# Kernel tuning notes

Hardware: AMD Instinct MI355X
Metric: run time of the kernel (lower is better)

The kernel has to match this reference:

```python
import jax, jax.numpy as jnp
import numpy as np

BATCH, SEQ, D_IN, D_OUT = 32, 1024, 128, 128
NEG_SLOPE = 0.1


def setup_inputs() -> dict:
    key = jax.random.key(0)
    k1, k2, k3, k4 = jax.random.split(key, 4)
    nodes = jax.random.normal(k1, (BATCH, SEQ, D_IN), dtype=jnp.float32)
    adjacent = jax.random.randint(k2, (BATCH, SEQ, SEQ), 0, 2, dtype=jnp.int32)
    W = jax.random.normal(k3, (D_IN, D_OUT), dtype=jnp.float32) / np.sqrt(D_IN)
    B = jax.random.normal(k4, (D_IN, D_OUT), dtype=jnp.float32) / np.sqrt(D_IN)
    return {"nodes": nodes, "adjacent": adjacent, "W": W, "B": B}


def reference(nodes, adjacent, W, B):
    # mask[b, out, in] = 1 if edge (out -> in) present
    mask = (adjacent != 0).astype(nodes.dtype)
    # counts[b, in] = in-degree (number of 'out' neighbors pooled per target node)
    counts = mask.sum(axis=1)                               # [b, s_in]
    # segment-sum of neighbor features: pooled[b, in, d] = sum_out mask * nodes[b, out, d]
    pooled = jnp.einsum('boi,bod->bid', mask, nodes)        # [b, s_in, d]
    # mean over neighbors; nodes with zero degree get no pooled contribution
    pooled = jnp.where(counts[..., None] > 0,
                       pooled / jnp.maximum(counts, 1.0)[..., None],
                       jnp.zeros((), dtype=nodes.dtype))
    updated = nodes @ B + pooled @ W                        # [b, s, d_out]
    return jax.nn.leaky_relu(updated, negative_slope=NEG_SLOPE)
```

## Files before the change

kernel.cpp:

```cpp
#include <hip/hip_runtime.h>
#include <hip/hip_bf16.h>

#define SEQ 1024
#define DIM 128
#define NEG_SLOPE 0.1f

typedef __bf16 bf16x8 __attribute__((ext_vector_type(8)));
typedef float f32x4v __attribute__((ext_vector_type(4)));

__device__ __forceinline__ unsigned short bfb(float f) {
    __bf16 h = (__bf16)f;
    return __builtin_bit_cast(unsigned short, h);
}
__device__ __forceinline__ unsigned mpack(int x0, int x1) {
    unsigned m0 = (x0 != 0) ? 0x3F80u : 0u;
    unsigned m1 = (x1 != 0) ? 0x3F80u : 0u;
    return m0 | (m1 << 16);
}
__device__ __forceinline__ int fxv(int x) {
    return ((x & 3) | ((x & 1) << 2)) ^ ((x >> 2) & 7);
}
__device__ __forceinline__ void bar() {
    asm volatile("s_waitcnt lgkmcnt(0)" ::: "memory");
    __builtin_amdgcn_s_barrier();
    __builtin_amdgcn_sched_barrier(0);
}

__global__ __launch_bounds__(256)
void wb_t(const float* __restrict__ W, const float* __restrict__ Bm,
          unsigned short* __restrict__ WT, unsigned short* __restrict__ BT) {
    const int gid = blockIdx.x * 256 + threadIdx.x;
    const int n = gid >> 7, k = gid & 127;
    WT[gid] = bfb(W[k * DIM + n]);
    BT[gid] = bfb(Bm[k * DIM + n]);
}

__global__ __launch_bounds__(256)
void nodes_t_kernel(const float* __restrict__ nodes, unsigned short* __restrict__ nodesT) {
    const int b  = blockIdx.x >> 4;
    const int o0 = (blockIdx.x & 15) << 6;
    __shared__ unsigned short T[DIM][66];

    const float* src = nodes + (size_t)b * SEQ * DIM;
    const int t = threadIdx.x & 31;
    const int g = threadIdx.x >> 5;

    float4 v[8];
    #pragma unroll
    for (int r = 0; r < 8; ++r)
        v[r] = *(const float4*)(src + (size_t)(o0 + g * 8 + r) * DIM + 4 * t);
    #pragma unroll
    for (int j = 0; j < 4; ++j) {
        #pragma unroll
        for (int p = 0; p < 4; ++p) {
            unsigned w = (unsigned)bfb(((const float*)&v[2 * p])[j]) |
                         ((unsigned)bfb(((const float*)&v[2 * p + 1])[j]) << 16);
            *(unsigned*)((unsigned char*)&T[0][0] + (size_t)(4 * t + j) * 132 + (g * 8 + 2 * p) * 2) = w;
        }
    }
    __syncthreads();
    const int d = threadIdx.x >> 1, h = threadIdx.x & 1;
    unsigned u[16];
    #pragma unroll
    for (int s = 0; s < 16; ++s)
        u[s] = *(const unsigned*)((const unsigned char*)&T[0][0] + (size_t)d * 132 + h * 64 + s * 4);
    unsigned short* dst = nodesT + (size_t)b * DIM * SEQ + (size_t)d * SEQ + o0 + h * 32;
    #pragma unroll
    for (int s = 0; s < 4; ++s) {
        uint4 q = make_uint4(u[4 * s], u[4 * s + 1], u[4 * s + 2], u[4 * s + 3]);
        *(uint4*)((unsigned char*)dst + s * 16) = q;
    }
}

__global__ __launch_bounds__(256, 4)
void gcn_fused(const float* __restrict__ nodes,
               const int* __restrict__ adj,
               const unsigned short* __restrict__ nodesT,
               const unsigned short* __restrict__ WT,
               const unsigned short* __restrict__ BT,
               float* __restrict__ out)
{
    __shared__ union {
        unsigned char  m[2][4096];
        unsigned short pooled[32][136];
    } u;

    const int bid   = blockIdx.x;
    const int xcd   = bid & 7;
    const int slot  = bid >> 3;
    const int batch = ((slot >> 5) << 3) | xcd;
    const int itile = slot & 31;
    const int i0    = itile << 5;

    const int tid  = threadIdx.x;
    const int wave = tid >> 6;
    const int lane = tid & 63;
    const int lrow = lane & 15;
    const int quad = lane >> 4;

    const int*            __restrict__ adj_b   = adj    + (size_t)batch * SEQ * SEQ;
    const float*          __restrict__ nodes_b = nodes  + (size_t)batch * SEQ * DIM;
    const unsigned short* __restrict__ nT_b    = nodesT + (size_t)batch * DIM * SEQ;

    const int tq   = tid >> 3;
    const int ic   = tid & 7;
    const int fxic = fxv(ic);
    const int gi0  = i0 + 4 * ic;
    const int o0   = 2 * tq;

    const int fx0 = fxv(lrow >> 2);
    const int fx1 = fxv(4 + (lrow >> 2));

    f32x4v acc[2][2] = {};
    f32x4v acc_cnt[2] = {};
    bf16x8 ones;
    #pragma unroll
    for (int j = 0; j < 8; ++j) ones[j] = __builtin_bit_cast(__bf16, (unsigned short)0x3F80);

    int4   A0[2], A1[2];
    bf16x8 bvA[4], bvB[4];

    auto load_adj = [&](int c, int4 (&A)[2]) {
        const int* pa = adj_b + (size_t)(c * 64 + o0) * SEQ + gi0;
        A[0] = *(const int4*)pa;
        A[1] = *(const int4*)(pa + SEQ);
    };
    auto load_bv = [&](int c, bf16x8 (&bv)[4]) {
        const unsigned short* pn = nT_b + (size_t)(wave * 32 + lrow) * SEQ + c * 64 + quad * 8;
        bv[0] = *(const bf16x8*)(pn);
        bv[1] = *(const bf16x8*)(pn + 16 * SEQ);
        bv[2] = *(const bf16x8*)(pn + 32);
        bv[3] = *(const bf16x8*)(pn + 16 * SEQ + 32);
    };
    auto write_mask = [&](int b, const int4 (&A)[2]) {
        unsigned char* mb = u.m[b];
        #pragma unroll
        for (int j = 0; j < 4; ++j) {
            unsigned w = mpack(((const int*)&A[0])[j], ((const int*)&A[1])[j]);
            *(unsigned*)(mb + (4 * ic + j) * 128 + (((tq >> 2) ^ fxic) << 4) + 4 * (tq & 3)) = w;
        }
    };
    auto compute = [&](int b, const bf16x8 (&bv)[4]) {
        const unsigned char* mb = u.m[b];
        #pragma unroll
        for (int kk = 0; kk < 2; ++kk) {
            bf16x8 av0 = *(const bf16x8*)(mb + lrow * 128        + (((4 * kk + quad) ^ fx0) << 4));
            bf16x8 av1 = *(const bf16x8*)(mb + (16 + lrow) * 128 + (((4 * kk + quad) ^ fx1) << 4));
            acc[0][0] = __builtin_amdgcn_mfma_f32_16x16x32_bf16(av0, bv[2 * kk + 0], acc[0][0], 0, 0, 0);
            acc[0][1] = __builtin_amdgcn_mfma_f32_16x16x32_bf16(av0, bv[2 * kk + 1], acc[0][1], 0, 0, 0);
            acc[1][0] = __builtin_amdgcn_mfma_f32_16x16x32_bf16(av1, bv[2 * kk + 0], acc[1][0], 0, 0, 0);
            acc[1][1] = __builtin_amdgcn_mfma_f32_16x16x32_bf16(av1, bv[2 * kk + 1], acc[1][1], 0, 0, 0);
            acc_cnt[0] = __builtin_amdgcn_mfma_f32_16x16x32_bf16(av0, ones, acc_cnt[0], 0, 0, 0);
            acc_cnt[1] = __builtin_amdgcn_mfma_f32_16x16x32_bf16(av1, ones, acc_cnt[1], 0, 0, 0);
        }
    };

    load_adj(0, A0); load_adj(1, A1);
    load_bv(0, bvA); load_bv(1, bvB);
    write_mask(0, A0);
    load_adj(2, A0);
    bar();

    for (int cc = 0; cc < 8; ++cc) {
        const int c0 = 2 * cc;
        compute(0, bvA);
        write_mask(1, A1);
        if (c0 + 3 < 16) load_adj(c0 + 3, A1);
        if (c0 + 2 < 16) load_bv(c0 + 2, bvA);
        bar();
        compute(1, bvB);
        if (c0 + 2 < 16) write_mask(0, A0);
        if (c0 + 4 < 16) load_adj(c0 + 4, A0);
        if (c0 + 3 < 16) load_bv(c0 + 3, bvB);
        bar();
    }

    #pragma unroll
    for (int mf = 0; mf < 2; ++mf) {
        #pragma unroll
        for (int r = 0; r < 4; ++r) {
            const int row = mf * 16 + quad * 4 + r;
            const float cnt = acc_cnt[mf][r];
            const float inv = (cnt > 0.5f) ? 1.0f / cnt : 0.0f;
            #pragma unroll
            for (int nf = 0; nf < 2; ++nf)
                u.pooled[row][wave * 32 + nf * 16 + lrow] = bfb(acc[mf][nf][r] * inv);
        }
    }
    bar();

    f32x4v acc2[2][2] = {};
    const int dn = wave * 32 + lrow;

    #pragma unroll
    for (int ks = 0; ks < 4; ++ks) {
        const int k0 = ks * 32 + quad * 8;
        bf16x8 av[2], bv2[2];
        #pragma unroll
        for (int mf = 0; mf < 2; ++mf)
            av[mf] = *(const bf16x8*)((const unsigned char*)&u.pooled[0][0] + (mf * 16 + lrow) * 272 + k0 * 2);
        #pragma unroll
        for (int nf = 0; nf < 2; ++nf)
            bv2[nf] = *(const bf16x8*)(WT + (size_t)(dn + nf * 16) * DIM + k0);
        #pragma unroll
        for (int mf = 0; mf < 2; ++mf)
            #pragma unroll
            for (int nf = 0; nf < 2; ++nf)
                acc2[mf][nf] = __builtin_amdgcn_mfma_f32_16x16x32_bf16(av[mf], bv2[nf], acc2[mf][nf], 0, 0, 0);
    }
    #pragma unroll
    for (int ks = 0; ks < 4; ++ks) {
        const int k0 = ks * 32 + quad * 8;
        bf16x8 av[2], bv2[2];
        #pragma unroll
        for (int mf = 0; mf < 2; ++mf) {
            const float* p = nodes_b + (size_t)(i0 + mf * 16 + lrow) * DIM + k0;
            const float4 f1 = *(const float4*)p;
            const float4 f2 = *(const float4*)(p + 4);
            av[mf][0] = (__bf16)f1.x; av[mf][1] = (__bf16)f1.y;
            av[mf][2] = (__bf16)f1.z; av[mf][3] = (__bf16)f1.w;
            av[mf][4] = (__bf16)f2.x; av[mf][5] = (__bf16)f2.y;
            av[mf][6] = (__bf16)f2.z; av[mf][7] = (__bf16)f2.w;
        }
        #pragma unroll
        for (int nf = 0; nf < 2; ++nf)
            bv2[nf] = *(const bf16x8*)(BT + (size_t)(dn + nf * 16) * DIM + k0);
        #pragma unroll
        for (int mf = 0; mf < 2; ++mf)
            #pragma unroll
            for (int nf = 0; nf < 2; ++nf)
                acc2[mf][nf] = __builtin_amdgcn_mfma_f32_16x16x32_bf16(av[mf], bv2[nf], acc2[mf][nf], 0, 0, 0);
    }

    float* out_b = out + (size_t)batch * SEQ * DIM;
    #pragma unroll
    for (int mf = 0; mf < 2; ++mf) {
        #pragma unroll
        for (int nf = 0; nf < 2; ++nf) {
            const int col = wave * 32 + nf * 16 + lrow;
            #pragma unroll
            for (int r = 0; r < 4; ++r) {
                const int row = i0 + mf * 16 + quad * 4 + r;
                const float x = acc2[mf][nf][r];
                out_b[(size_t)row * DIM + col] = (x > 0.0f) ? x : NEG_SLOPE * x;
            }
        }
    }
}

#define BUF_STRIDE 24576
#define NODES_OFF  8192
__device__ __forceinline__ int fb_swz(int row, int unit) {
    const int x  = row >> 2;
    const int fx = ((x & 3) | ((x & 1) << 2)) ^ ((x >> 2) & 7);
    return row * 128 + ((unit ^ fx) << 4);
}
__global__ __launch_bounds__(256, 2)
void gcn_fused_fb(const float* __restrict__ nodes, const int* __restrict__ adj,
                  const float* __restrict__ W, const float* __restrict__ Bm,
                  float* __restrict__ out)
{
    __shared__ alignas(16) unsigned char lds[2 * BUF_STRIDE];
    const int bid = blockIdx.x, xcd = bid & 7, slot = bid >> 3;
    const int batch = ((slot >> 4) << 3) | xcd, mtile = slot & 15, i0 = mtile << 6;
    const int tid = threadIdx.x, wave = tid >> 6, lane = tid & 63;
    const int wm = wave >> 1, wn = wave & 1, lrow = lane & 15, quad = lane >> 4;
    const int* __restrict__ adj_b = adj + (size_t)batch * SEQ * SEQ;
    const float* __restrict__ nodes_b = nodes + (size_t)batch * SEQ * DIM;
    const int a_row = (tid >> 4) * 4, a_col = (tid & 15) * 4;
    const int n_row = (tid >> 5) * 4, n_col = (tid & 31) * 4;
    const int m_unit = (tid >> 4) >> 1, m_sub = ((tid >> 4) & 1) * 8;
    const int n_unit = (tid >> 5) >> 1, n_sub = ((tid >> 5) & 1) * 8;
    f32x4v acc[2][4] = {}; f32x4v acc_cnt[2] = {};
    bf16x8 ones;
    #pragma unroll
    for (int j = 0; j < 8; ++j) ones[j] = __builtin_bit_cast(__bf16, (unsigned short)0x3F80);
    int4 A0[4], A1[4]; float4 N0[8], N1[8];
    auto load_chunk = [&](int o0, int4 (&A)[4], float4 (&N)[8]) {
        const int* pa = adj_b + (size_t)(o0 + a_row) * SEQ + (i0 + a_col);
        #pragma unroll
        for (int r = 0; r < 4; ++r) A[r] = *(const int4*)(pa + (size_t)r * SEQ);
        const float* pn = nodes_b + (size_t)(o0 + n_row) * DIM + n_col;
        #pragma unroll
        for (int it = 0; it < 2; ++it)
            #pragma unroll
            for (int r = 0; r < 4; ++r)
                N[it * 4 + r] = *(const float4*)(pn + (size_t)(it * 32 + r) * DIM);
    };
    auto write_lds = [&](int base, const int4 (&A)[4], const float4 (&N)[8]) {
        unsigned char* mb = lds + base; unsigned char* nb = lds + base + NODES_OFF;
        #pragma unroll
        for (int j = 0; j < 4; ++j) {
            uint2 w;
            w.x = mpack(((const int*)&A[0])[j], ((const int*)&A[1])[j]);
            w.y = mpack(((const int*)&A[2])[j], ((const int*)&A[3])[j]);
            *(uint2*)(mb + fb_swz(a_col + j, m_unit) + m_sub) = w;
        }
        #pragma unroll
        for (int it = 0; it < 2; ++it) {
            #pragma unroll
            for (int j = 0; j < 4; ++j) {
                uint2 w;
                w.x = (unsigned)bfb(((const float*)&N[it*4+0])[j]) | ((unsigned)bfb(((const float*)&N[it*4+1])[j]) << 16);
                w.y = (unsigned)bfb(((const float*)&N[it*4+2])[j]) | ((unsigned)bfb(((const float*)&N[it*4+3])[j]) << 16);
                *(uint2*)(nb + fb_swz(n_col + j, 4 * it + n_unit) + n_sub) = w;
            }
        }
    };
    auto compute = [&](int base) {
        const unsigned char* mb = lds + base; const unsigned char* nb = lds + base + NODES_OFF;
        #pragma unroll
        for (int kk = 0; kk < 2; ++kk) {
            bf16x8 av[2], bv[4];
            av[0] = *(const bf16x8*)(mb + fb_swz(wm * 32 + lrow, 4 * kk + quad));
            av[1] = *(const bf16x8*)(mb + fb_swz(wm * 32 + 16 + lrow, 4 * kk + quad));
            #pragma unroll
            for (int nf = 0; nf < 4; ++nf)
                bv[nf] = *(const bf16x8*)(nb + fb_swz(wn * 64 + nf * 16 + lrow, 4 * kk + quad));
            #pragma unroll
            for (int mf = 0; mf < 2; ++mf) {
                #pragma unroll
                for (int nf = 0; nf < 4; ++nf)
                    acc[mf][nf] = __builtin_amdgcn_mfma_f32_16x16x32_bf16(av[mf], bv[nf], acc[mf][nf], 0, 0, 0);
                acc_cnt[mf] = __builtin_amdgcn_mfma_f32_16x16x32_bf16(av[mf], ones, acc_cnt[mf], 0, 0, 0);
            }
        }
    };
    load_chunk(0, A0, N0); load_chunk(64, A1, N1);
    write_lds(0, A0, N0); load_chunk(128, A0, N0); bar();
    for (int cc = 0; cc < 8; ++cc) {
        const int c0 = cc * 2;
        compute(0); write_lds(BUF_STRIDE, A1, N1);
        if (c0 + 3 < 16) load_chunk((c0 + 3) * 64, A1, N1);
        bar();
        compute(BUF_STRIDE);
        if (c0 + 2 < 16) write_lds(0, A0, N0);
        if (c0 + 4 < 16) load_chunk((c0 + 4) * 64, A0, N0);
        bar();
    }
    unsigned short (*pooled)[136] = (unsigned short (*)[136])(void*)lds;
    #pragma unroll
    for (int mf = 0; mf < 2; ++mf)
        #pragma unroll
        for (int r = 0; r < 4; ++r) {
            const int row = wm * 32 + mf * 16 + quad * 4 + r;
            const float cnt = acc_cnt[mf][r];
            const float inv = (cnt > 0.5f) ? 1.0f / cnt : 0.0f;
            #pragma unroll
            for (int nf = 0; nf < 4; ++nf)
                pooled[row][wn * 64 + nf * 16 + lrow] = bfb(acc[mf][nf][r] * inv);
        }
    __syncthreads();
    f32x4v acc2[2][4] = {};
    const int d_b0 = wn * 64 + lrow;
    #pragma unroll
    for (int ks = 0; ks < 4; ++ks) {
        const int k0 = ks * 32 + quad * 8;
        bf16x8 av[2];
        #pragma unroll
        for (int mf = 0; mf < 2; ++mf)
            av[mf] = *(const bf16x8*)&pooled[wm * 32 + mf * 16 + lrow][k0];
        bf16x8 bv[4];
        const float* pw = W + (size_t)k0 * DIM + d_b0;
        #pragma unroll
        for (int nf = 0; nf < 4; ++nf)
            #pragma unroll
            for (int j = 0; j < 8; ++j) bv[nf][j] = (__bf16)pw[j * DIM + nf * 16];
        #pragma unroll
        for (int mf = 0; mf < 2; ++mf)
            #pragma unroll
            for (int nf = 0; nf < 4; ++nf)
                acc2[mf][nf] = __builtin_amdgcn_mfma_f32_16x16x32_bf16(av[mf], bv[nf], acc2[mf][nf], 0, 0, 0);
    }
    #pragma unroll
    for (int ks = 0; ks < 4; ++ks) {
        const int k0 = ks * 32 + quad * 8;
        bf16x8 av[2];
        #pragma unroll
        for (int mf = 0; mf < 2; ++mf) {
            const float* p = nodes_b + (size_t)(i0 + wm * 32 + mf * 16 + lrow) * DIM + k0;
            const float4 f1 = *(const float4*)p; const float4 f2 = *(const float4*)(p + 4);
            av[mf][0] = (__bf16)f1.x; av[mf][1] = (__bf16)f1.y;
            av[mf][2] = (__bf16)f1.z; av[mf][3] = (__bf16)f1.w;
            av[mf][4] = (__bf16)f2.x; av[mf][5] = (__bf16)f2.y;
            av[mf][6] = (__bf16)f2.z; av[mf][7] = (__bf16)f2.w;
        }
        bf16x8 bv[4];
        const float* pB = Bm + (size_t)k0 * DIM + d_b0;
        #pragma unroll
        for (int nf = 0; nf < 4; ++nf)
            #pragma unroll
            for (int j = 0; j < 8; ++j) bv[nf][j] = (__bf16)pB[j * DIM + nf * 16];
        #pragma unroll
        for (int mf = 0; mf < 2; ++mf)
            #pragma unroll
            for (int nf = 0; nf < 4; ++nf)
                acc2[mf][nf] = __builtin_amdgcn_mfma_f32_16x16x32_bf16(av[mf], bv[nf], acc2[mf][nf], 0, 0, 0);
    }
    float* out_b = out + (size_t)batch * SEQ * DIM;
    #pragma unroll
    for (int mf = 0; mf < 2; ++mf)
        #pragma unroll
        for (int nf = 0; nf < 4; ++nf) {
            const int col = wn * 64 + nf * 16 + lrow;
            #pragma unroll
            for (int r = 0; r < 4; ++r) {
                const int row = i0 + wm * 32 + mf * 16 + quad * 4 + r;
                const float x = acc2[mf][nf][r];
                out_b[(size_t)row * DIM + col] = (x > 0.0f) ? x : NEG_SLOPE * x;
            }
        }
}

extern "C" void kernel_launch(void* const* d_in, const int* in_sizes, int n_in,
                              void* d_out, int out_size, void* d_ws, size_t ws_size,
                              hipStream_t stream) {
    const float* nodes = (const float*)d_in[0];
    const int*   adj   = (const int*)d_in[1];
    const float* W     = (const float*)d_in[2];
    const float* Bm    = (const float*)d_in[3];
    float*       out   = (float*)d_out;

    const size_t NT_BYTES = (size_t)32 * DIM * SEQ * 2;
    const size_t WB_BYTES = (size_t)DIM * DIM * 2;
    const size_t NEED = NT_BYTES + 2 * WB_BYTES;

    if (d_ws != nullptr && ws_size >= NEED) {
        unsigned short* nodesT = (unsigned short*)d_ws;
        unsigned short* WT = (unsigned short*)((char*)d_ws + NT_BYTES);
        unsigned short* BT = (unsigned short*)((char*)d_ws + NT_BYTES + WB_BYTES);
        wb_t<<<dim3(64), dim3(256), 0, stream>>>(W, Bm, WT, BT);
        nodes_t_kernel<<<dim3(512), dim3(256), 0, stream>>>(nodes, nodesT);
        gcn_fused<<<dim3(1024), dim3(256), 0, stream>>>(nodes, adj, nodesT, WT, BT, out);
    } else {
        gcn_fused_fb<<<dim3(512), dim3(256), 0, stream>>>(nodes, adj, W, Bm, out);
    }
}
```

Baseline: 240.3 us.

## Pre-pack adjacency into bitmasks and expand mask operands in registers

Adds an adj_pack kernel that reads the int32 adjacency once and writes a transposed per-tile bitmask, one 32-bit word per (batch, i-tile, out-node). The fused GCN kernel then loads these compact words and expands the bits into bf16 MFMA A-operands in registers. This removes the LDS mask staging, its swizzle, and the two barriers per step in the main loop. In exchange it adds a kernel launch, an extra pass over the 128 MB adjacency with a workspace write, and more ALU work per MFMA for bit expansion.

```diff
diff --git a/kernel.cpp b/kernel.cpp
--- a/kernel.cpp
+++ b/kernel.cpp
@@ -16,9 +16,6 @@
     unsigned m0 = (x0 != 0) ? 0x3F80u : 0u;
     unsigned m1 = (x1 != 0) ? 0x3F80u : 0u;
     return m0 | (m1 << 16);
-}
-__device__ __forceinline__ int fxv(int x) {
-    return ((x & 3) | ((x & 1) << 2)) ^ ((x >> 2) & 7);
 }
 __device__ __forceinline__ void bar() {
     asm volatile("s_waitcnt lgkmcnt(0)" ::: "memory");
@@ -72,18 +69,52 @@
     }
 }
 
+__global__ __launch_bounds__(256)
+void adj_pack(const int* __restrict__ adj, unsigned* __restrict__ packT) {
+    const int b  = blockIdx.x >> 5;
+    const int o0 = (blockIdx.x & 31) << 5;
+    const int t = threadIdx.x;
+    const int itile = t >> 3;
+    const int oq    = t & 7;
+    const int* src = adj + (size_t)b * SEQ * SEQ + (size_t)itile * 32;
+    unsigned w[4];
+    #pragma unroll
+    for (int oo = 0; oo < 4; ++oo) {
+        const int o = o0 + oq * 4 + oo;
+        const int* p = src + (size_t)o * SEQ;
+        unsigned bits = 0;
+        #pragma unroll
+        for (int r = 0; r < 8; ++r) {
+            int4 v = *(const int4*)(p + r * 4);
+            bits |= (v.x != 0 ? 1u : 0u) << (r * 4 + 0);
+            bits |= (v.y != 0 ? 1u : 0u) << (r * 4 + 1);
+            bits |= (v.z != 0 ? 1u : 0u) << (r * 4 + 2);
+            bits |= (v.w != 0 ? 1u : 0u) << (r * 4 + 3);
+        }
+        w[oo] = bits;
+    }
+    unsigned* dst = packT + (size_t)b * 32 * SEQ + (size_t)itile * SEQ + o0 + oq * 4;
+    *(uint4*)dst = make_uint4(w[0], w[1], w[2], w[3]);
+}
+
+__device__ __forceinline__ bf16x8 expand8(const uint4 Wa, const uint4 Wb, int s) {
+    union { unsigned u[4]; bf16x8 v; } r;
+    r.u[0] = ((Wa.x >> s) & 1u) * 0x3F80u | ((((Wa.y >> s) & 1u) * 0x3F80u) << 16);
+    r.u[1] = ((Wa.z >> s) & 1u) * 0x3F80u | ((((Wa.w >> s) & 1u) * 0x3F80u) << 16);
+    r.u[2] = ((Wb.x >> s) & 1u) * 0x3F80u | ((((Wb.y >> s) & 1u) * 0x3F80u) << 16);
+    r.u[3] = ((Wb.z >> s) & 1u) * 0x3F80u | ((((Wb.w >> s) & 1u) * 0x3F80u) << 16);
+    return r.v;
+}
+
 __global__ __launch_bounds__(256, 4)
 void gcn_fused(const float* __restrict__ nodes,
-               const int* __restrict__ adj,
+               const unsigned* __restrict__ packT,
                const unsigned short* __restrict__ nodesT,
                const unsigned short* __restrict__ WT,
                const unsigned short* __restrict__ BT,
                float* __restrict__ out)
 {
-    __shared__ union {
-        unsigned char  m[2][4096];
-        unsigned short pooled[32][136];
-    } u;
+    __shared__ unsigned short pooled[32][136];
 
     const int bid   = blockIdx.x;
     const int xcd   = bid & 7;
@@ -98,18 +129,9 @@
     const int lrow = lane & 15;
     const int quad = lane >> 4;
 
-    const int*            __restrict__ adj_b   = adj    + (size_t)batch * SEQ * SEQ;
     const float*          __restrict__ nodes_b = nodes  + (size_t)batch * SEQ * DIM;
+    const unsigned*       __restrict__ pk_b    = packT  + (size_t)batch * 32 * SEQ + (size_t)itile * SEQ;
     const unsigned short* __restrict__ nT_b    = nodesT + (size_t)batch * DIM * SEQ;
-
-    const int tq   = tid >> 3;
-    const int ic   = tid & 7;
-    const int fxic = fxv(ic);
-    const int gi0  = i0 + 4 * ic;
-    const int o0   = 2 * tq;
-
-    const int fx0 = fxv(lrow >> 2);
-    const int fx1 = fxv(4 + (lrow >> 2));
 
     f32x4v acc[2][2] = {};
     f32x4v acc_cnt[2] = {};
@@ -117,13 +139,15 @@
     #pragma unroll
     for (int j = 0; j < 8; ++j) ones[j] = __builtin_bit_cast(__bf16, (unsigned short)0x3F80);
 
-    int4   A0[2], A1[2];
+    uint4  PA[4], PB[4];
     bf16x8 bvA[4], bvB[4];
 
-    auto load_adj = [&](int c, int4 (&A)[2]) {
-        const int* pa = adj_b + (size_t)(c * 64 + o0) * SEQ + gi0;
-        A[0] = *(const int4*)pa;
-        A[1] = *(const int4*)(pa + SEQ);
+    auto load_pk = [&](int c, uint4 (&P)[4]) {
+        const unsigned* p = pk_b + c * 64 + quad * 8;
+        P[0] = *(const uint4*)p;
+        P[1] = *(const uint4*)(p + 4);
+        P[2] = *(const uint4*)(p + 32);
+        P[3] = *(const uint4*)(p + 36);
     };
     auto load_bv = [&](int c, bf16x8 (&bv)[4]) {
         const unsigned short* pn = nT_b + (size_t)(wave * 32 + lrow) * SEQ + c * 64 + quad * 8;
@@ -132,20 +156,11 @@
         bv[2] = *(const bf16x8*)(pn + 32);
         bv[3] = *(const bf16x8*)(pn + 16 * SEQ + 32);
     };
-    auto write_mask = [&](int b, const int4 (&A)[2]) {
-        unsigned char* mb = u.m[b];
-        #pragma unroll
-        for (int j = 0; j < 4; ++j) {
-            unsigned w = mpack(((const int*)&A[0])[j], ((const int*)&A[1])[j]);
-            *(unsigned*)(mb + (4 * ic + j) * 128 + (((tq >> 2) ^ fxic) << 4) + 4 * (tq & 3)) = w;
-        }
-    };
-    auto compute = [&](int b, const bf16x8 (&bv)[4]) {
-        const unsigned char* mb = u.m[b];
+    auto compute = [&](const uint4 (&P)[4], const bf16x8 (&bv)[4]) {
         #pragma unroll
         for (int kk = 0; kk < 2; ++kk) {
-            bf16x8 av0 = *(const bf16x8*)(mb + lrow * 128        + (((4 * kk + quad) ^ fx0) << 4));
-            bf16x8 av1 = *(const bf16x8*)(mb + (16 + lrow) * 128 + (((4 * kk + quad) ^ fx1) << 4));
+            bf16x8 av0 = expand8(P[2 * kk], P[2 * kk + 1], lrow);
+            bf16x8 av1 = expand8(P[2 * kk], P[2 * kk + 1], lrow + 16);
             acc[0][0] = __builtin_amdgcn_mfma_f32_16x16x32_bf16(av0, bv[2 * kk + 0], acc[0][0], 0, 0, 0);
             acc[0][1] = __builtin_amdgcn_mfma_f32_16x16x32_bf16(av0, bv[2 * kk + 1], acc[0][1], 0, 0, 0);
             acc[1][0] = __builtin_amdgcn_mfma_f32_16x16x32_bf16(av1, bv[2 * kk + 0], acc[1][0], 0, 0, 0);
@@ -155,24 +170,14 @@
         }
     };
 
-    load_adj(0, A0); load_adj(1, A1);
-    load_bv(0, bvA); load_bv(1, bvB);
-    write_mask(0, A0);
-    load_adj(2, A0);
-    bar();
-
+    load_pk(0, PA); load_bv(0, bvA);
+    load_pk(1, PB); load_bv(1, bvB);
     for (int cc = 0; cc < 8; ++cc) {
         const int c0 = 2 * cc;
-        compute(0, bvA);
-        write_mask(1, A1);
-        if (c0 + 3 < 16) load_adj(c0 + 3, A1);
-        if (c0 + 2 < 16) load_bv(c0 + 2, bvA);
-        bar();
-        compute(1, bvB);
-        if (c0 + 2 < 16) write_mask(0, A0);
-        if (c0 + 4 < 16) load_adj(c0 + 4, A0);
-        if (c0 + 3 < 16) load_bv(c0 + 3, bvB);
-        bar();
+        compute(PA, bvA);
+        if (c0 + 2 < 16) { load_pk(c0 + 2, PA); load_bv(c0 + 2, bvA); }
+        compute(PB, bvB);
+        if (c0 + 3 < 16) { load_pk(c0 + 3, PB); load_bv(c0 + 3, bvB); }
     }
 
     #pragma unroll
@@ -184,7 +189,7 @@
             const float inv = (cnt > 0.5f) ? 1.0f / cnt : 0.0f;
             #pragma unroll
             for (int nf = 0; nf < 2; ++nf)
-                u.pooled[row][wave * 32 + nf * 16 + lrow] = bfb(acc[mf][nf][r] * inv);
+                pooled[row][wave * 32 + nf * 16 + lrow] = bfb(acc[mf][nf][r] * inv);
         }
     }
     bar();
@@ -198,7 +203,7 @@
         bf16x8 av[2], bv2[2];
         #pragma unroll
         for (int mf = 0; mf < 2; ++mf)
-            av[mf] = *(const bf16x8*)((const unsigned char*)&u.pooled[0][0] + (mf * 16 + lrow) * 272 + k0 * 2);
+            av[mf] = *(const bf16x8*)((const unsigned char*)&pooled[0][0] + (mf * 16 + lrow) * 272 + k0 * 2);
         #pragma unroll
         for (int nf = 0; nf < 2; ++nf)
             bv2[nf] = *(const bf16x8*)(WT + (size_t)(dn + nf * 16) * DIM + k0);
@@ -421,17 +426,20 @@
     const float* Bm    = (const float*)d_in[3];
     float*       out   = (float*)d_out;
 
+    const size_t PK_BYTES = (size_t)32 * 32 * SEQ * 4;
     const size_t NT_BYTES = (size_t)32 * DIM * SEQ * 2;
     const size_t WB_BYTES = (size_t)DIM * DIM * 2;
-    const size_t NEED = NT_BYTES + 2 * WB_BYTES;
+    const size_t NEED = PK_BYTES + NT_BYTES + 2 * WB_BYTES;
 
     if (d_ws != nullptr && ws_size >= NEED) {
-        unsigned short* nodesT = (unsigned short*)d_ws;
-        unsigned short* WT = (unsigned short*)((char*)d_ws + NT_BYTES);
-        unsigned short* BT = (unsigned short*)((char*)d_ws + NT_BYTES + WB_BYTES);
+        unsigned*       packT  = (unsigned*)d_ws;
+        unsigned short* nodesT = (unsigned short*)((char*)d_ws + PK_BYTES);
+        unsigned short* WT = (unsigned short*)((char*)d_ws + PK_BYTES + NT_BYTES);
+        unsigned short* BT = (unsigned short*)((char*)d_ws + PK_BYTES + NT_BYTES + WB_BYTES);
         wb_t<<<dim3(64), dim3(256), 0, stream>>>(W, Bm, WT, BT);
         nodes_t_kernel<<<dim3(512), dim3(256), 0, stream>>>(nodes, nodesT);
-        gcn_fused<<<dim3(1024), dim3(256), 0, stream>>>(nodes, adj, nodesT, WT, BT, out);
+        adj_pack<<<dim3(1024), dim3(256), 0, stream>>>(adj, packT);
+        gcn_fused<<<dim3(1024), dim3(256), 0, stream>>>(nodes, packT, nodesT, WT, BT, out);
     } else {
         gcn_fused_fb<<<dim3(512), dim3(256), 0, stream>>>(nodes, adj, W, Bm, out);
     }
```

Measured after the change: 278.3 us. +15.8%, slower.
